# Kernel tuning notes

Hardware: AMD Instinct MI355X
Metric: run time of the kernel (lower is better)

The kernel has to match this reference:

```python
import jax, jax.numpy as jnp
import numpy as np


def _layernorm(x, g, b, eps=1e-5):
    mu = jnp.mean(x, axis=-1, keepdims=True)
    var = jnp.mean(jnp.square(x - mu), axis=-1, keepdims=True)
    return (x - mu) * jax.lax.rsqrt(var + eps) * g + b


def setup_inputs() -> dict:
    key = jax.random.key(0)
    ks = jax.random.split(key, 8)
    dim, ctx_dim, heads, dim_head = 256, 256, 8, 64
    inner = heads * dim_head
    s = 0.02
    return {
        "x": jax.random.normal(ks[0], (4, dim, 64, 64), jnp.float32),
        "y": jax.random.normal(ks[1], (4, 1024, ctx_dim), jnp.float32),
        "ln_x_g": jnp.ones((dim,), jnp.float32),
        "ln_x_b": jnp.zeros((dim,), jnp.float32),
        "ln_y_g": jnp.ones((ctx_dim,), jnp.float32),
        "ln_y_b": jnp.zeros((ctx_dim,), jnp.float32),
        "Wq": jax.random.normal(ks[2], (dim, inner), jnp.float32) * s,
        "Wk": jax.random.normal(ks[3], (ctx_dim, inner), jnp.float32) * s,
        "Wv": jax.random.normal(ks[4], (ctx_dim, inner), jnp.float32) * s,
        "bv": jnp.zeros((inner,), jnp.float32),
        "Wo": jax.random.normal(ks[5], (inner, dim), jnp.float32) * s,
        "bo": jnp.zeros((dim,), jnp.float32),
    }


def reference(x, y, ln_x_g, ln_x_b, ln_y_g, ln_y_b, Wq, Wk, Wv, bv, Wo, bo):
    heads, dim_head = 8, 64
    b, c = x.shape[:2]
    # channel_last=False path: [b, c, H, W] -> [b, n, c]
    xn = x.reshape(b, c, -1).swapaxes(1, 2)
    xn = _layernorm(xn, ln_x_g, ln_x_b)          # note: x is reassigned in torch code
    yn = _layernorm(y, ln_y_g, ln_y_b)
    q = xn @ Wq                                   # [b, n, h*d]
    k = yn @ Wk                                   # [b, m, h*d]
    v = yn @ Wv + bv                              # [b, m, h*d]

    def split_heads(t):
        B, N, _ = t.shape
        return t.reshape(B, N, heads, dim_head).transpose(0, 2, 1, 3)  # [b, h, n, d]

    q, k, v = split_heads(q), split_heads(k), split_heads(v)
    attn = jnp.einsum("bhid,bhjd->bhij", q, k) * (dim_head ** -0.5)
    attn = jax.nn.softmax(attn, axis=-1)
    out = jnp.einsum("bhij,bhjd->bhid", attn, v)  # [b, h, n, d]
    out = out.transpose(0, 2, 1, 3).reshape(b, -1, heads * dim_head)
    out = out @ Wo + bo
    return xn + out  # residual with layernormed x (faithful to source)
```

## Files before the change

### kernel.cpp

```cpp
#include <hip/hip_runtime.h>
#include <hip/hip_bf16.h>
#include <cstddef>
#include <cstdint>

#define BATCH 4
#define CDIM 256
#define HW 4096
#define MCTX 1024
#define CTX 256
#define HEADS 8
#define DHEAD 64
#define INNER 512

typedef __attribute__((ext_vector_type(8))) short bf16x8;
typedef __attribute__((ext_vector_type(4))) float f32x4;

static __device__ __forceinline__ ushort f2bf(float f) {
  __hip_bfloat16 h = __float2bfloat16(f);
  return *reinterpret_cast<ushort*>(&h);
}

static __device__ __forceinline__ void gload16(const void* g, void* l) {
  __builtin_amdgcn_global_load_lds(
      (const __attribute__((address_space(1))) void*)(uintptr_t)g,
      (__attribute__((address_space(3))) void*)(uint32_t)(uintptr_t)l,
      16, 0, 0);
}

__global__ __launch_bounds__(256) void ln_x_kernel(
    const float* __restrict__ x, const float* __restrict__ g,
    const float* __restrict__ bta, float* __restrict__ xn,
    ushort* __restrict__ xnbf) {
  const int blk = blockIdx.x;
  const int bi = blk / (HW / 32);
  const int n0 = (blk % (HW / 32)) * 32;
  __shared__ float xt[32][257];
  __shared__ float smu[32], srs[32];
  const int t = threadIdx.x;
  const int nl = t & 31;
  const int c0 = t >> 5;
  const float* xb = x + (size_t)bi * CDIM * HW;
  #pragma unroll
  for (int c = c0; c < CDIM; c += 8)
    xt[nl][c] = xb[(size_t)c * HW + n0 + nl];
  __syncthreads();
  const int col = t >> 3, j = t & 7;
  float s = 0.f, ss = 0.f;
  #pragma unroll
  for (int c = j; c < CDIM; c += 8) {
    float v = xt[col][c];
    s += v; ss += v * v;
  }
  #pragma unroll
  for (int off = 1; off < 8; off <<= 1) {
    s += __shfl_xor(s, off);
    ss += __shfl_xor(ss, off);
  }
  if (j == 0) {
    float mu = s * (1.f / CDIM);
    smu[col] = mu;
    srs[col] = rsqrtf(ss * (1.f / CDIM) - mu * mu + 1e-5f);
  }
  __syncthreads();
  const float gv = g[t], bvv = bta[t];
  float* xnb = xn + ((size_t)bi * HW + n0) * CDIM;
  ushort* xbb = xnbf + ((size_t)bi * HW + n0) * CDIM;
  #pragma unroll 4
  for (int n = 0; n < 32; ++n) {
    float val = (xt[n][t] - smu[n]) * srs[n] * gv + bvv;
    xnb[(size_t)n * CDIM + t] = val;
    xbb[(size_t)n * CDIM + t] = f2bf(val);
  }
}

__global__ __launch_bounds__(256) void ln_y_kernel(
    const float* __restrict__ y, const float* __restrict__ g,
    const float* __restrict__ bta, ushort* __restrict__ ynbf) {
  const int row = blockIdx.x * 4 + (threadIdx.x >> 6);
  const int t = threadIdx.x & 63;
  float4 v = ((const float4*)(y + (size_t)row * CTX))[t];
  float s = v.x + v.y + v.z + v.w;
  float ss = v.x * v.x + v.y * v.y + v.z * v.z + v.w * v.w;
  #pragma unroll
  for (int off = 1; off < 64; off <<= 1) {
    s += __shfl_xor(s, off);
    ss += __shfl_xor(ss, off);
  }
  float mu = s * (1.f / CTX);
  float rs = rsqrtf(ss * (1.f / CTX) - mu * mu + 1e-5f);
  float4 gv = ((const float4*)g)[t];
  float4 b4 = ((const float4*)bta)[t];
  ushort4 ob;
  ob.x = f2bf((v.x - mu) * rs * gv.x + b4.x);
  ob.y = f2bf((v.y - mu) * rs * gv.y + b4.y);
  ob.z = f2bf((v.z - mu) * rs * gv.z + b4.z);
  ob.w = f2bf((v.w - mu) * rs * gv.w + b4.w);
  *(ushort4*)(ynbf + (size_t)row * CTX + t * 4) = ob;
}

static __device__ __forceinline__ void wprep_body(
    const float* __restrict__ W, ushort* __restrict__ Wt, int K, int N) {
  __shared__ ushort T[64][65];
  const int k0 = blockIdx.y * 64, n0 = blockIdx.x * 64;
  const int t = threadIdx.x;
  #pragma unroll
  for (int rr = 0; rr < 4; ++rr) {
    int row = rr * 16 + (t >> 4);
    int c = (t & 15) * 4;
    float4 wv = *(const float4*)(W + (size_t)(k0 + row) * N + n0 + c);
    T[row][c + 0] = f2bf(wv.x); T[row][c + 1] = f2bf(wv.y);
    T[row][c + 2] = f2bf(wv.z); T[row][c + 3] = f2bf(wv.w);
  }
  __syncthreads();
  #pragma unroll
  for (int rr = 0; rr < 4; ++rr) {
    int nrow = rr * 16 + (t >> 4);
    int kc = (t & 15) * 4;
    ushort4 o;
    o.x = T[kc + 0][nrow]; o.y = T[kc + 1][nrow];
    o.z = T[kc + 2][nrow]; o.w = T[kc + 3][nrow];
    *(ushort4*)(Wt + (size_t)(n0 + nrow) * K + k0 + kc) = o;
  }
}

__global__ __launch_bounds__(256) void wprep3_kernel(
    const float* __restrict__ W0, const float* __restrict__ W1,
    const float* __restrict__ W2, ushort* __restrict__ T0,
    ushort* __restrict__ T1, ushort* __restrict__ T2) {
  const int z = blockIdx.z;
  const float* W = (z == 0) ? W0 : (z == 1) ? W1 : W2;
  ushort* Wt = (z == 0) ? T0 : (z == 1) ? T1 : T2;
  wprep_body(W, Wt, 256, 512);
}

__global__ __launch_bounds__(256) void wprep_kernel(
    const float* __restrict__ W, ushort* __restrict__ Wt, int K, int N) {
  wprep_body(W, Wt, K, N);
}

__global__ __launch_bounds__(256) void vtr_kernel(
    const ushort* __restrict__ v, ushort* __restrict__ vt) {
  const int bh = blockIdx.z, bi = bh >> 3, h = bh & 7;
  const int m0 = blockIdx.x * 64;
  __shared__ ushort T[64][65];
  const int t = threadIdx.x;
  #pragma unroll
  for (int rr = 0; rr < 4; ++rr) {
    int row = rr * 16 + (t >> 4);
    int c = (t & 15) * 4;
    ushort4 vv = *(const ushort4*)(v + (size_t)(bi * MCTX + m0 + row) * INNER + h * DHEAD + c);
    T[row][c + 0] = vv.x; T[row][c + 1] = vv.y;
    T[row][c + 2] = vv.z; T[row][c + 3] = vv.w;
  }
  __syncthreads();
  #pragma unroll
  for (int rr = 0; rr < 4; ++rr) {
    int drow = rr * 16 + (t >> 4);
    int mc = (t & 15) * 4;
    ushort4 o;
    o.x = T[mc + 0][drow]; o.y = T[mc + 1][drow];
    o.z = T[mc + 2][drow]; o.w = T[mc + 3][drow];
    *(ushort4*)(vt + (size_t)(bh * 64 + drow) * MCTX + m0 + mc) = o;
  }
}

template <bool F32_RES_OUT>
static __device__ __forceinline__ void gemm_body(
    const ushort* __restrict__ A, const ushort* __restrict__ Bt,
    const float* __restrict__ bias, const float* __restrict__ res,
    void* __restrict__ Cout, int M, int N, int K, float scale,
    int m0, int n0) {
  __shared__ ushort As[128 * 64];
  __shared__ ushort Bs[128 * 64];
  const int t = threadIdx.x;
  const int l = t & 63, w = t >> 6;
  const int lq = l & 15, lg = l >> 4;
  const int wr = w >> 1, wc = w & 1;
  f32x4 acc[4][4];
  #pragma unroll
  for (int mt = 0; mt < 4; ++mt)
    #pragma unroll
    for (int nt = 0; nt < 4; ++nt)
      #pragma unroll
      for (int e = 0; e < 4; ++e) acc[mt][nt][e] = 0.f;
  const int srow = w * 8 + (l >> 3);
  const int scol = ((l & 7) ^ (l >> 3)) * 8;
  const ushort* pA = A + (size_t)(m0 + srow) * K + scol;
  const ushort* pB = Bt + (size_t)(n0 + srow) * K + scol;
  const int dbase = w * 512;
  for (int k0 = 0; k0 < K; k0 += 64) {
    if (k0) __syncthreads();
    #pragma unroll
    for (int i = 0; i < 4; ++i) {
      gload16(pA + (size_t)(i * 32) * K + k0, &As[i * 2048 + dbase]);
      gload16(pB + (size_t)(i * 32) * K + k0, &Bs[i * 2048 + dbase]);
    }
    __syncthreads();
    #pragma unroll
    for (int ks = 0; ks < 2; ++ks) {
      bf16x8 af[4], bfr[4];
      #pragma unroll
      for (int mt = 0; mt < 4; ++mt) {
        const int R = wr * 64 + mt * 16 + lq;
        af[mt] = *(const bf16x8*)(
            &As[R * 64 + ((ks * 32 + lg * 8) ^ ((R & 7) * 8))]);
      }
      #pragma unroll
      for (int nt = 0; nt < 4; ++nt) {
        const int R = wc * 64 + nt * 16 + lq;
        bfr[nt] = *(const bf16x8*)(
            &Bs[R * 64 + ((ks * 32 + lg * 8) ^ ((R & 7) * 8))]);
      }
      #pragma unroll
      for (int mt = 0; mt < 4; ++mt)
        #pragma unroll
        for (int nt = 0; nt < 4; ++nt)
          acc[mt][nt] = __builtin_amdgcn_mfma_f32_16x16x32_bf16(
              af[mt], bfr[nt], acc[mt][nt], 0, 0, 0);
    }
  }
  #pragma unroll
  for (int nt = 0; nt < 4; ++nt) {
    const int colc = n0 + wc * 64 + nt * 16 + lq;
    const float bcol = bias ? bias[colc] : 0.f;
    #pragma unroll
    for (int mt = 0; mt < 4; ++mt) {
      #pragma unroll
      for (int i = 0; i < 4; ++i) {
        const size_t row = (size_t)(m0 + wr * 64 + mt * 16 + lg * 4 + i);
        float v = acc[mt][nt][i] * scale + bcol;
        if (F32_RES_OUT) {
          ((float*)Cout)[row * N + colc] = v + res[row * N + colc];
        } else {
          ((ushort*)Cout)[row * N + colc] = f2bf(v);
        }
      }
    }
  }
}

template <bool F32_RES_OUT>
__global__ __launch_bounds__(256) void mfma_gemm(
    const ushort* __restrict__ A, const ushort* __restrict__ Bt,
    const float* __restrict__ bias, const float* __restrict__ res,
    void* __restrict__ Cout, int M, int N, int K, float scale) {
  gemm_body<F32_RES_OUT>(A, Bt, bias, res, Cout, M, N, K, scale,
                         blockIdx.y * 128, blockIdx.x * 128);
}

__global__ __launch_bounds__(256) void mfma_gemm_kv(
    const ushort* __restrict__ A, const ushort* __restrict__ BtK,
    const ushort* __restrict__ BtV, const float* __restrict__ bv,
    ushort* __restrict__ Ck, ushort* __restrict__ Cv) {
  const bool isV = blockIdx.x >= 4;
  gemm_body<false>(A, isV ? BtV : BtK, isV ? bv : nullptr, nullptr,
                   isV ? (void*)Cv : (void*)Ck, 4096, 512, 256, 1.f,
                   blockIdx.y * 128, (blockIdx.x & 3) * 128);
}

__global__ __launch_bounds__(512, 4) void attn_mfma(
    const ushort* __restrict__ q, const ushort* __restrict__ k,
    const ushort* __restrict__ vt, ushort* __restrict__ ao) {
  const int bid = blockIdx.x + 16 * (blockIdx.y + 8 * blockIdx.z);
  const int swz = (bid & 7) * 64 + (bid >> 3);
  const int bi = swz >> 7;
  const int h = (swz >> 4) & 7;
  const int n0 = (swz & 15) * 256;
  __shared__ ushort Ks[2][64 * 64];
  __shared__ ushort Vs[2][64 * 64];
  __shared__ ushort Ps[8][2][16 * 64];
  const int t = threadIdx.x;
  const int l = t & 63, w = t >> 6;
  const int lq = l & 15, lg = l >> 4;

  bf16x8 bq[2][2];
  #pragma unroll
  for (int g = 0; g < 2; ++g) {
    const size_t qrow = (size_t)(bi * HW + n0 + w * 32 + g * 16 + lq);
    #pragma unroll
    for (int ks = 0; ks < 2; ++ks)
      bq[g][ks] = *(const bf16x8*)(q + qrow * INNER + h * DHEAD + ks * 32 + lg * 8);
  }

  float m_run[2] = {-1e30f, -1e30f}, l_run[2] = {0.f, 0.f};
  f32x4 oacc[2][4];
  #pragma unroll
  for (int g = 0; g < 2; ++g)
    #pragma unroll
    for (int dt = 0; dt < 4; ++dt)
      #pragma unroll
      for (int e = 0; e < 4; ++e) oacc[g][dt][e] = 0.f;

  const int rr = t >> 3, cc = (t & 7) * 8;
  const ushort* kptr = k + (size_t)(bi * MCTX + rr) * INNER + h * DHEAD + cc;
  const ushort* vptr = vt + (size_t)((bi * HEADS + h) * 64 + rr) * MCTX + cc;
  const int sidx = (rr * 64 + cc) ^ ((rr & 7) << 3);

  {
    uint4 k0v = *(const uint4*)(kptr);
    uint4 v0v = *(const uint4*)(vptr);
    *(uint4*)(&Ks[0][sidx]) = k0v;
    *(uint4*)(&Vs[0][sidx]) = v0v;
  }
  __syncthreads();

  auto softmax_group = [&](f32x4 (&scg)[4], float& mr, float& lr,
                           f32x4 (&oa)[4], ushort* psw) {
    f32x4 mv;
    #pragma unroll
    for (int e = 0; e < 4; ++e)
      mv[e] = fmaxf(fmaxf(scg[0][e], scg[1][e]), fmaxf(scg[2][e], scg[3][e]));
    float mloc = fmaxf(fmaxf(mv[0], mv[1]), fmaxf(mv[2], mv[3]));
    mloc = fmaxf(mloc, __shfl_xor(mloc, 16));
    mloc = fmaxf(mloc, __shfl_xor(mloc, 32));
    if (!__all((int)(mloc - mr <= 8.f))) {
      const float mnew = fmaxf(mr, mloc);
      const float corr = __builtin_amdgcn_exp2f(mr - mnew);
      lr *= corr;
      mr = mnew;
      #pragma unroll
      for (int i = 0; i < 4; ++i) {
        float ci = __shfl(corr, lg * 4 + i);
        #pragma unroll
        for (int dt = 0; dt < 4; ++dt) oa[dt][i] *= ci;
      }
    }
    #pragma unroll
    for (int j = 0; j < 4; ++j)
      #pragma unroll
      for (int e = 0; e < 4; ++e)
        scg[j][e] = __builtin_amdgcn_exp2f(scg[j][e] - mr);
    f32x4 s4;
    #pragma unroll
    for (int e = 0; e < 4; ++e)
      s4[e] = (scg[0][e] + scg[1][e]) + (scg[2][e] + scg[3][e]);
    float psum = (s4[0] + s4[1]) + (s4[2] + s4[3]);
    psum += __shfl_xor(psum, 16);
    psum += __shfl_xor(psum, 32);
    lr += psum;
    #pragma unroll
    for (int j = 0; j < 4; ++j) {
      uint2 pk;
      pk.x = (uint)f2bf(scg[j][0]) | ((uint)f2bf(scg[j][1]) << 16);
      pk.y = (uint)f2bf(scg[j][2]) | ((uint)f2bf(scg[j][3]) << 16);
      *(uint2*)(psw + ((lq * 64 + j * 16 + lg * 4) ^ ((lq & 7) << 3))) = pk;
    }
  };

  #pragma unroll 2
  for (int m0 = 0; m0 < MCTX; m0 += 64) {
    const int buf = (m0 >> 6) & 1;
    const bool more = (m0 + 64) < MCTX;
    uint4 kpre{}, vpre{};
    if (more) {
      kpre = *(const uint4*)(kptr + (size_t)(m0 + 64) * INNER);
      vpre = *(const uint4*)(vptr + (m0 + 64));
    }
    f32x4 sc[2][4];
    #pragma unroll
    for (int g = 0; g < 2; ++g)
      #pragma unroll
      for (int j = 0; j < 4; ++j)
        #pragma unroll
        for (int e = 0; e < 4; ++e) sc[g][j][e] = 0.f;
    __builtin_amdgcn_s_setprio(1);
    #pragma unroll
    for (int j = 0; j < 4; ++j) {
      #pragma unroll
      for (int ks = 0; ks < 2; ++ks) {
        const int krow = j * 16 + lq;
        bf16x8 ak = *(const bf16x8*)(
            &Ks[buf][(krow * 64 + ks * 32 + lg * 8) ^ ((krow & 7) << 3)]);
        sc[0][j] = __builtin_amdgcn_mfma_f32_16x16x32_bf16(ak, bq[0][ks], sc[0][j], 0, 0, 0);
        sc[1][j] = __builtin_amdgcn_mfma_f32_16x16x32_bf16(ak, bq[1][ks], sc[1][j], 0, 0, 0);
      }
    }
    __builtin_amdgcn_s_setprio(0);
    softmax_group(sc[0], m_run[0], l_run[0], oacc[0], &Ps[w][0][0]);
    if (more) {
      *(uint4*)(&Ks[buf ^ 1][sidx]) = kpre;
      *(uint4*)(&Vs[buf ^ 1][sidx]) = vpre;
    }
    softmax_group(sc[1], m_run[1], l_run[1], oacc[1], &Ps[w][1][0]);
    bf16x8 pa[2][2];
    #pragma unroll
    for (int g = 0; g < 2; ++g)
      #pragma unroll
      for (int ks = 0; ks < 2; ++ks)
        pa[g][ks] = *(const bf16x8*)(
            &Ps[w][g][(lq * 64 + ks * 32 + lg * 8) ^ ((lq & 7) << 3)]);
    __builtin_amdgcn_s_setprio(1);
    #pragma unroll
    for (int dt = 0; dt < 4; ++dt) {
      #pragma unroll
      for (int ks = 0; ks < 2; ++ks) {
        const int vrow = dt * 16 + lq;
        bf16x8 vb = *(const bf16x8*)(
            &Vs[buf][(vrow * 64 + ks * 32 + lg * 8) ^ ((vrow & 7) << 3)]);
        oacc[0][dt] = __builtin_amdgcn_mfma_f32_16x16x32_bf16(pa[0][ks], vb, oacc[0][dt], 0, 0, 0);
        oacc[1][dt] = __builtin_amdgcn_mfma_f32_16x16x32_bf16(pa[1][ks], vb, oacc[1][dt], 0, 0, 0);
      }
    }
    __builtin_amdgcn_s_setprio(0);
    __syncthreads();
  }
  #pragma unroll
  for (int g = 0; g < 2; ++g) {
    const float rl = 1.f / l_run[g];
    #pragma unroll
    for (int i = 0; i < 4; ++i) {
      float li = __shfl(rl, lg * 4 + i);
      const size_t row = (size_t)(bi * HW + n0 + w * 32 + g * 16 + lg * 4 + i);
      #pragma unroll
      for (int dt = 0; dt < 4; ++dt)
        ao[row * INNER + h * DHEAD + dt * 16 + lq] = f2bf(oacc[g][dt][i] * li);
    }
  }
}

extern "C" void kernel_launch(void* const* d_in, const int* in_sizes, int n_in,
                              void* d_out, int out_size, void* d_ws, size_t ws_size,
                              hipStream_t stream) {
  const float* x     = (const float*)d_in[0];
  const float* y     = (const float*)d_in[1];
  const float* ln_xg = (const float*)d_in[2];
  const float* ln_xb = (const float*)d_in[3];
  const float* ln_yg = (const float*)d_in[4];
  const float* ln_yb = (const float*)d_in[5];
  const float* Wq    = (const float*)d_in[6];
  const float* Wk    = (const float*)d_in[7];
  const float* Wv    = (const float*)d_in[8];
  const float* bv    = (const float*)d_in[9];
  const float* Wo    = (const float*)d_in[10];
  const float* bo    = (const float*)d_in[11];
  float* out = (float*)d_out;

  char* p = (char*)d_ws;
  float*  xn   = (float*)p;  p += (size_t)16384 * 256 * 4;
  ushort* xnbf = (ushort*)p; p += (size_t)16384 * 256 * 2;
  ushort* ynbf = (ushort*)p; p += (size_t)4096 * 256 * 2;
  ushort* wtq  = (ushort*)p; p += (size_t)512 * 256 * 2;
  ushort* wtk  = (ushort*)p; p += (size_t)512 * 256 * 2;
  ushort* wtv  = (ushort*)p; p += (size_t)512 * 256 * 2;
  ushort* wto  = (ushort*)p; p += (size_t)256 * 512 * 2;
  ushort* qbf  = (ushort*)p; p += (size_t)16384 * 512 * 2;
  ushort* kbf  = (ushort*)p; p += (size_t)4096 * 512 * 2;
  ushort* vbf  = (ushort*)p; p += (size_t)4096 * 512 * 2;
  ushort* vtb  = (ushort*)p; p += (size_t)4096 * 512 * 2;
  ushort* aobf = (ushort*)p; p += (size_t)16384 * 512 * 2;

  wprep3_kernel<<<dim3(8, 4, 3), 256, 0, stream>>>(Wq, Wk, Wv, wtq, wtk, wtv);
  wprep_kernel<<<dim3(4, 8), 256, 0, stream>>>(Wo, wto, 512, 256);
  ln_x_kernel<<<dim3(BATCH * (HW / 32)), 256, 0, stream>>>(x, ln_xg, ln_xb, xn, xnbf);
  ln_y_kernel<<<dim3(BATCH * MCTX / 4), 256, 0, stream>>>(y, ln_yg, ln_yb, ynbf);
  mfma_gemm<false><<<dim3(4, 128), 256, 0, stream>>>(
      xnbf, wtq, nullptr, nullptr, qbf, 16384, 512, 256, 0.1803368801111204f);
  mfma_gemm_kv<<<dim3(8, 32), 256, 0, stream>>>(ynbf, wtk, wtv, bv, kbf, vbf);
  vtr_kernel<<<dim3(16, 1, 32), 256, 0, stream>>>(vbf, vtb);
  attn_mfma<<<dim3(HW / 256, HEADS, BATCH), 512, 0, stream>>>(qbf, kbf, vtb, aobf);
  mfma_gemm<true><<<dim3(2, 128), 256, 0, stream>>>(
      aobf, wto, bo, xn, out, 16384, 256, 512, 1.f);
}
```

Measured before the change: 119.1 us.

## Fuse V transpose into KV GEMM, stagger attention KV tiles, vectorize LN loads

The KV projection GEMM now writes V directly in the transposed per-head layout, which removes the separate transpose kernel and the intermediate V buffer. Attention blocks start their K/V tile loop at a block-dependent offset, so concurrent blocks read different tiles of the same head instead of all hitting the same one. The x layernorm loads float4 per thread instead of scalars. The transposed-V store from the GEMM epilogue is strided, so those writes are poorly coalesced.

```diff
diff --git a/kernel.cpp b/kernel.cpp
--- a/kernel.cpp
+++ b/kernel.cpp
@@ -37,12 +37,18 @@
   __shared__ float xt[32][257];
   __shared__ float smu[32], srs[32];
   const int t = threadIdx.x;
-  const int nl = t & 31;
-  const int c0 = t >> 5;
   const float* xb = x + (size_t)bi * CDIM * HW;
-  #pragma unroll
-  for (int c = c0; c < CDIM; c += 8)
-    xt[nl][c] = xb[(size_t)c * HW + n0 + nl];
+  {
+    const int cr = t >> 3;
+    const int n4 = (t & 7) * 4;
+    #pragma unroll
+    for (int pass = 0; pass < 8; ++pass) {
+      const int c = pass * 32 + cr;
+      float4 v = *(const float4*)(xb + (size_t)c * HW + n0 + n4);
+      xt[n4 + 0][c] = v.x; xt[n4 + 1][c] = v.y;
+      xt[n4 + 2][c] = v.z; xt[n4 + 3][c] = v.w;
+    }
+  }
   __syncthreads();
   const int col = t >> 3, j = t & 7;
   float s = 0.f, ss = 0.f;
@@ -138,38 +144,12 @@
   wprep_body(W, Wt, K, N);
 }
 
-__global__ __launch_bounds__(256) void vtr_kernel(
-    const ushort* __restrict__ v, ushort* __restrict__ vt) {
-  const int bh = blockIdx.z, bi = bh >> 3, h = bh & 7;
-  const int m0 = blockIdx.x * 64;
-  __shared__ ushort T[64][65];
-  const int t = threadIdx.x;
-  #pragma unroll
-  for (int rr = 0; rr < 4; ++rr) {
-    int row = rr * 16 + (t >> 4);
-    int c = (t & 15) * 4;
-    ushort4 vv = *(const ushort4*)(v + (size_t)(bi * MCTX + m0 + row) * INNER + h * DHEAD + c);
-    T[row][c + 0] = vv.x; T[row][c + 1] = vv.y;
-    T[row][c + 2] = vv.z; T[row][c + 3] = vv.w;
-  }
-  __syncthreads();
-  #pragma unroll
-  for (int rr = 0; rr < 4; ++rr) {
-    int drow = rr * 16 + (t >> 4);
-    int mc = (t & 15) * 4;
-    ushort4 o;
-    o.x = T[mc + 0][drow]; o.y = T[mc + 1][drow];
-    o.z = T[mc + 2][drow]; o.w = T[mc + 3][drow];
-    *(ushort4*)(vt + (size_t)(bh * 64 + drow) * MCTX + m0 + mc) = o;
-  }
-}
-
 template <bool F32_RES_OUT>
 static __device__ __forceinline__ void gemm_body(
     const ushort* __restrict__ A, const ushort* __restrict__ Bt,
     const float* __restrict__ bias, const float* __restrict__ res,
-    void* __restrict__ Cout, int M, int N, int K, float scale,
-    int m0, int n0) {
+    void* __restrict__ Cout, ushort* __restrict__ vt_out,
+    int M, int N, int K, float scale, int m0, int n0) {
   __shared__ ushort As[128 * 64];
   __shared__ ushort Bs[128 * 64];
   const int t = threadIdx.x;
@@ -229,7 +209,10 @@
       for (int i = 0; i < 4; ++i) {
         const size_t row = (size_t)(m0 + wr * 64 + mt * 16 + lg * 4 + i);
         float v = acc[mt][nt][i] * scale + bcol;
-        if (F32_RES_OUT) {
+        if (vt_out) {
+          vt_out[(size_t)((((row >> 10) * 8 + (colc >> 6)) << 6) + (colc & 63)) * MCTX
+                 + (row & (MCTX - 1))] = f2bf(v);
+        } else if (F32_RES_OUT) {
           ((float*)Cout)[row * N + colc] = v + res[row * N + colc];
         } else {
           ((ushort*)Cout)[row * N + colc] = f2bf(v);
@@ -244,17 +227,17 @@
     const ushort* __restrict__ A, const ushort* __restrict__ Bt,
     const float* __restrict__ bias, const float* __restrict__ res,
     void* __restrict__ Cout, int M, int N, int K, float scale) {
-  gemm_body<F32_RES_OUT>(A, Bt, bias, res, Cout, M, N, K, scale,
+  gemm_body<F32_RES_OUT>(A, Bt, bias, res, Cout, nullptr, M, N, K, scale,
                          blockIdx.y * 128, blockIdx.x * 128);
 }
 
 __global__ __launch_bounds__(256) void mfma_gemm_kv(
     const ushort* __restrict__ A, const ushort* __restrict__ BtK,
     const ushort* __restrict__ BtV, const float* __restrict__ bv,
-    ushort* __restrict__ Ck, ushort* __restrict__ Cv) {
+    ushort* __restrict__ Ck, ushort* __restrict__ vt_out) {
   const bool isV = blockIdx.x >= 4;
   gemm_body<false>(A, isV ? BtV : BtK, isV ? bv : nullptr, nullptr,
-                   isV ? (void*)Cv : (void*)Ck, 4096, 512, 256, 1.f,
+                   (void*)Ck, isV ? vt_out : nullptr, 4096, 512, 256, 1.f,
                    blockIdx.y * 128, (blockIdx.x & 3) * 128);
 }
 
@@ -266,6 +249,7 @@
   const int bi = swz >> 7;
   const int h = (swz >> 4) & 7;
   const int n0 = (swz & 15) * 256;
+  const int tile0 = (bid & 3) << 2;
   __shared__ ushort Ks[2][64 * 64];
   __shared__ ushort Vs[2][64 * 64];
   __shared__ ushort Ps[8][2][16 * 64];
@@ -297,8 +281,9 @@
   const int sidx = (rr * 64 + cc) ^ ((rr & 7) << 3);
 
   {
-    uint4 k0v = *(const uint4*)(kptr);
-    uint4 v0v = *(const uint4*)(vptr);
+    const int ms = tile0 << 6;
+    uint4 k0v = *(const uint4*)(kptr + (size_t)ms * INNER);
+    uint4 v0v = *(const uint4*)(vptr + ms);
     *(uint4*)(&Ks[0][sidx]) = k0v;
     *(uint4*)(&Vs[0][sidx]) = v0v;
   }
@@ -348,13 +333,14 @@
   };
 
   #pragma unroll 2
-  for (int m0 = 0; m0 < MCTX; m0 += 64) {
-    const int buf = (m0 >> 6) & 1;
-    const bool more = (m0 + 64) < MCTX;
+  for (int it = 0; it < 16; ++it) {
+    const int buf = it & 1;
+    const bool more = (it + 1) < 16;
+    const int mnext = ((tile0 + it + 1) & 15) << 6;
     uint4 kpre{}, vpre{};
     if (more) {
-      kpre = *(const uint4*)(kptr + (size_t)(m0 + 64) * INNER);
-      vpre = *(const uint4*)(vptr + (m0 + 64));
+      kpre = *(const uint4*)(kptr + (size_t)mnext * INNER);
+      vpre = *(const uint4*)(vptr + mnext);
     }
     f32x4 sc[2][4];
     #pragma unroll
@@ -445,7 +431,6 @@
   ushort* wto  = (ushort*)p; p += (size_t)256 * 512 * 2;
   ushort* qbf  = (ushort*)p; p += (size_t)16384 * 512 * 2;
   ushort* kbf  = (ushort*)p; p += (size_t)4096 * 512 * 2;
-  ushort* vbf  = (ushort*)p; p += (size_t)4096 * 512 * 2;
   ushort* vtb  = (ushort*)p; p += (size_t)4096 * 512 * 2;
   ushort* aobf = (ushort*)p; p += (size_t)16384 * 512 * 2;
 
@@ -455,8 +440,7 @@
   ln_y_kernel<<<dim3(BATCH * MCTX / 4), 256, 0, stream>>>(y, ln_yg, ln_yb, ynbf);
   mfma_gemm<false><<<dim3(4, 128), 256, 0, stream>>>(
       xnbf, wtq, nullptr, nullptr, qbf, 16384, 512, 256, 0.1803368801111204f);
-  mfma_gemm_kv<<<dim3(8, 32), 256, 0, stream>>>(ynbf, wtk, wtv, bv, kbf, vbf);
-  vtr_kernel<<<dim3(16, 1, 32), 256, 0, stream>>>(vbf, vtb);
+  mfma_gemm_kv<<<dim3(8, 32), 256, 0, stream>>>(ynbf, wtk, wtv, bv, kbf, vtb);
   attn_mfma<<<dim3(HW / 256, HEADS, BATCH), 512, 0, stream>>>(qbf, kbf, vtb, aobf);
   mfma_gemm<true><<<dim3(2, 128), 256, 0, stream>>>(
       aobf, wto, bo, xn, out, 16384, 256, 512, 1.f);
```

After: 116.7 us. 2.0% less time.
